# Kernel tuning notes

Hardware: AMD Instinct MI355X
Metric: run time of the kernel (lower is better)

The kernel has to match this reference:

```python
import jax, jax.numpy as jnp
import numpy as np

EPS = 1e-6  # module eps (unused in forward math, kept for fidelity)


def _relative_transform(rot_a, trans_a, rot_b, trans_b):
    # rel_rot = R_a @ R_b^T ; rel_trans = t_a - rel_rot @ t_b
    rel_rot = jnp.einsum('bij,bkj->bik', rot_a, rot_b)          # [B,3,3]
    rel_trans = trans_a - jnp.einsum('bij,bj->bi', rel_rot, trans_b)  # [B,3]
    return rel_rot, rel_trans


def setup_inputs() -> dict:
    key = jax.random.key(0)
    ks = jax.random.split(key, 9)
    B, N = 8, 4096
    return {
        'pred_rot': jax.random.normal(ks[0], (B, 3, 3), jnp.float32),
        'pred_trans': jax.random.normal(ks[1], (B, 3), jnp.float32),
        'ctx_hyp_rot': jax.random.normal(ks[2], (B, 3, 3), jnp.float32),
        'ctx_hyp_trans': jax.random.normal(ks[3], (B, 3), jnp.float32),
        'gt_rot': jax.random.normal(ks[4], (B, 3, 3), jnp.float32),
        'gt_trans': jax.random.normal(ks[5], (B, 3), jnp.float32),
        'ctx_gt_rot': jax.random.normal(ks[6], (B, 3, 3), jnp.float32),
        'ctx_gt_trans': jax.random.normal(ks[7], (B, 3), jnp.float32),
        'model_points': jax.random.normal(ks[8], (B, N, 3), jnp.float32),
    }


def reference(pred_rot, pred_trans, ctx_hyp_rot, ctx_hyp_trans,
              gt_rot, gt_trans, ctx_gt_rot, ctx_gt_trans, model_points):
    rel_pred_rot, rel_pred_trans = _relative_transform(pred_rot, pred_trans, ctx_hyp_rot, ctx_hyp_trans)
    rel_gt_rot, rel_gt_trans = _relative_transform(gt_rot, gt_trans, ctx_gt_rot, ctx_gt_trans)

    # pts = P @ R^T + t   -> [B,N,3]
    pts_pred = jnp.einsum('bnj,bij->bni', model_points, rel_pred_rot) + rel_pred_trans[:, None, :]
    pts_gt = jnp.einsum('bnj,bij->bni', model_points, rel_gt_rot) + rel_gt_trans[:, None, :]

    # pairwise euclidean distance [B,N,M]
    sq = (jnp.sum(pts_pred**2, -1)[:, :, None]
          + jnp.sum(pts_gt**2, -1)[:, None, :]
          - 2.0 * jnp.einsum('bnd,bmd->bnm', pts_pred, pts_gt))
    dist = jnp.sqrt(jnp.maximum(sq, 0.0))

    # symmetric chamfer: mean of row-min + mean of col-min, per batch
    loss_geo = jnp.min(dist, axis=2).mean(axis=1) + jnp.min(dist, axis=1).mean(axis=1)  # [B]
    loss_trans = jnp.abs(rel_pred_trans - rel_gt_trans).mean()
    return (loss_geo.mean(), loss_trans)
```

## Files before the change

kernel.cpp:

```cpp
#include <hip/hip_runtime.h>
#include <hip/hip_bf16.h>
#include <math.h>


#define TPB 256
#define RPT 8
#define MC  128
#define RC  (TPB * RPT)

__device__ __forceinline__ unsigned f2ord(float f) {
    unsigned u = __float_as_uint(f);
    return (u & 0x80000000u) ? ~u : (u | 0x80000000u);
}
__device__ __forceinline__ float ord2f(unsigned u) {
    return (u & 0x80000000u) ? __uint_as_float(u & 0x7fffffffu)
                             : __uint_as_float(~u);
}

__device__ __forceinline__ void rel_tf(const float* __restrict__ Ra,
                                       const float* __restrict__ ta,
                                       const float* __restrict__ Rb,
                                       const float* __restrict__ tb,
                                       float* R, float* t) {
#pragma unroll
    for (int i = 0; i < 3; i++)
#pragma unroll
        for (int k = 0; k < 3; k++)
            R[i * 3 + k] = Ra[i * 3 + 0] * Rb[k * 3 + 0]
                         + Ra[i * 3 + 1] * Rb[k * 3 + 1]
                         + Ra[i * 3 + 2] * Rb[k * 3 + 2];
#pragma unroll
    for (int i = 0; i < 3; i++)
        t[i] = ta[i] - (R[i * 3 + 0] * tb[0] + R[i * 3 + 1] * tb[1]
                      + R[i * 3 + 2] * tb[2]);
}

__global__ void k_prep(const float* __restrict__ pred_rot,
                       const float* __restrict__ pred_trans,
                       const float* __restrict__ ctx_hyp_rot,
                       const float* __restrict__ ctx_hyp_trans,
                       const float* __restrict__ gt_rot,
                       const float* __restrict__ gt_trans,
                       const float* __restrict__ ctx_gt_rot,
                       const float* __restrict__ ctx_gt_trans,
                       const float* __restrict__ mp,
                       float4* __restrict__ pts,
                       unsigned* __restrict__ rowmin,
                       float* __restrict__ out, int B, int N) {
    int idx = blockIdx.x * blockDim.x + threadIdx.x;
    if (idx >= B * N) return;
    int b = idx / N;
    float px = mp[idx * 3 + 0], py = mp[idx * 3 + 1], pz = mp[idx * 3 + 2];
    float R[9], t[3];
#pragma unroll
    for (int g = 0; g < 2; g++) {
        if (g == 0)
            rel_tf(pred_rot + b * 9, pred_trans + b * 3,
                   ctx_hyp_rot + b * 9, ctx_hyp_trans + b * 3, R, t);
        else
            rel_tf(gt_rot + b * 9, gt_trans + b * 3,
                   ctx_gt_rot + b * 9, ctx_gt_trans + b * 3, R, t);
        float x = R[0] * px + R[1] * py + R[2] * pz + t[0];
        float y = R[3] * px + R[4] * py + R[5] * pz + t[1];
        float z = R[6] * px + R[7] * py + R[8] * pz + t[2];
        pts[(size_t)g * B * N + idx] = make_float4(x, y, z, x * x + y * y + z * z);
    }
    rowmin[idx] = 0xFFFFFFFFu;
    rowmin[(size_t)B * N + idx] = 0xFFFFFFFFu;
    if (idx == 0) {
        out[0] = 0.0f;
        float lt = 0.0f;
        for (int bb = 0; bb < B; bb++) {
            float Rp[9], tp[3], Rg[9], tg[3];
            rel_tf(pred_rot + bb * 9, pred_trans + bb * 3,
                   ctx_hyp_rot + bb * 9, ctx_hyp_trans + bb * 3, Rp, tp);
            rel_tf(gt_rot + bb * 9, gt_trans + bb * 3,
                   ctx_gt_rot + bb * 9, ctx_gt_trans + bb * 3, Rg, tg);
            lt += fabsf(tp[0] - tg[0]) + fabsf(tp[1] - tg[1]) + fabsf(tp[2] - tg[2]);
        }
        out[1] = lt / (float)(3 * B);
    }
}

__global__ void __launch_bounds__(TPB) k_chamfer(const float4* __restrict__ pts,
                                                 unsigned* __restrict__ rowmin,
                                                 int B, int N) {
    int dir = blockIdx.z;
    int b = blockIdx.y;
    int nMC = N / MC;
    int rc = blockIdx.x / nMC;
    int mc = blockIdx.x % nMC;
    const float4* Ap = pts + ((size_t)dir * B + b) * N;
    const float4* Bp = pts + ((size_t)(1 - dir) * B + b) * N;

    __shared__ float4 sB[MC];
    int tid = threadIdx.x;
    for (int i = tid; i < MC; i += TPB) sB[i] = Bp[mc * MC + i];

    int rowBase = rc * RC;
    float a2x[RPT], a2y[RPT], a2z[RPT], mn[RPT];
#pragma unroll
    for (int r = 0; r < RPT; r++) {
        float4 a = Ap[rowBase + tid + TPB * r];
        a2x[r] = -2.0f * a.x;
        a2y[r] = -2.0f * a.y;
        a2z[r] = -2.0f * a.z;
        mn[r] = INFINITY;
    }
    __syncthreads();

#pragma unroll 4
    for (int m = 0; m < MC; m++) {
        float4 g = sB[m];
#pragma unroll
        for (int r = 0; r < RPT; r++) {
            float p = __builtin_fmaf(a2z[r], g.z, g.w);
            p = __builtin_fmaf(a2y[r], g.y, p);
            p = __builtin_fmaf(a2x[r], g.x, p);
            mn[r] = fminf(mn[r], p);
        }
    }

#pragma unroll
    for (int r = 0; r < RPT; r++) {
        size_t idx = ((size_t)dir * B + b) * N + rowBase + tid + TPB * r;
        atomicMin(&rowmin[idx], f2ord(mn[r]));
    }
}

__global__ void k_finalize(const float4* __restrict__ pts,
                           const unsigned* __restrict__ rowmin,
                           float* __restrict__ out, int B, int N) {
    int total = 2 * B * N;
    float s = 0.0f;
    for (int i = blockIdx.x * blockDim.x + threadIdx.x; i < total;
         i += gridDim.x * blockDim.x) {
        float part = ord2f(rowmin[i]);
        float sq = fmaxf(part + pts[i].w, 0.0f);
        s += sqrtf(sq);
    }
#pragma unroll
    for (int off = 32; off > 0; off >>= 1) s += __shfl_down(s, off, 64);
    __shared__ float red[TPB / 64];
    int wid = threadIdx.x >> 6, lane = threadIdx.x & 63;
    if (lane == 0) red[wid] = s;
    __syncthreads();
    if (threadIdx.x == 0) {
        float t = 0.0f;
#pragma unroll
        for (int w = 0; w < TPB / 64; w++) t += red[w];
        atomicAdd(&out[0], t / (float)(B * N));
    }
}

extern "C" void kernel_launch(void* const* d_in, const int* in_sizes, int n_in,
                              void* d_out, int out_size, void* d_ws, size_t ws_size,
                              hipStream_t stream) {
    const float* pred_rot      = (const float*)d_in[0];
    const float* pred_trans    = (const float*)d_in[1];
    const float* ctx_hyp_rot   = (const float*)d_in[2];
    const float* ctx_hyp_trans = (const float*)d_in[3];
    const float* gt_rot        = (const float*)d_in[4];
    const float* gt_trans      = (const float*)d_in[5];
    const float* ctx_gt_rot    = (const float*)d_in[6];
    const float* ctx_gt_trans  = (const float*)d_in[7];
    const float* model_points  = (const float*)d_in[8];

    int B = in_sizes[0] / 9;
    int N = in_sizes[8] / (3 * B);

    char* ws = (char*)d_ws;
    float4*   pts    = (float4*)ws;
    unsigned* rowmin = (unsigned*)(ws + (size_t)2 * B * N * 16);
    float*    out    = (float*)d_out;

    k_prep<<<(B * N + TPB - 1) / TPB, TPB, 0, stream>>>(
        pred_rot, pred_trans, ctx_hyp_rot, ctx_hyp_trans,
        gt_rot, gt_trans, ctx_gt_rot, ctx_gt_trans,
        model_points, pts, rowmin, out, B, N);

    dim3 grid((N / RC) * (N / MC), B, 2);
    k_chamfer<<<grid, TPB, 0, stream>>>(pts, rowmin, B, N);

    k_finalize<<<128, TPB, 0, stream>>>(pts, rowmin, out, B, N);
}
```

Before: 97.21 us.

## Fuse both chamfer directions into one pass with row and column partial minima

Each pairwise distance tile is now computed once and reduced both ways. Row minima stay in registers, while column minima are reduced across the wavefront with xor shuffles and across waves in shared memory. This removes the duplicate second-direction pass and the atomicMin on order-encoded floats. Per-tile partial minima are written to workspace buffers and combined in the finalize kernel. The cost is extra shuffle traffic per column pair, a smaller column tile, and a larger partial buffer that finalize must read.

```diff
diff --git a/kernel.cpp b/kernel.cpp
--- a/kernel.cpp
+++ b/kernel.cpp
@@ -1,21 +1,11 @@
 #include <hip/hip_runtime.h>
-#include <hip/hip_bf16.h>
 #include <math.h>
 
 
 #define TPB 256
 #define RPT 8
-#define MC  128
+#define MC  64
 #define RC  (TPB * RPT)
-
-__device__ __forceinline__ unsigned f2ord(float f) {
-    unsigned u = __float_as_uint(f);
-    return (u & 0x80000000u) ? ~u : (u | 0x80000000u);
-}
-__device__ __forceinline__ float ord2f(unsigned u) {
-    return (u & 0x80000000u) ? __uint_as_float(u & 0x7fffffffu)
-                             : __uint_as_float(~u);
-}
 
 __device__ __forceinline__ void rel_tf(const float* __restrict__ Ra,
                                        const float* __restrict__ ta,
@@ -45,7 +35,6 @@
                        const float* __restrict__ ctx_gt_trans,
                        const float* __restrict__ mp,
                        float4* __restrict__ pts,
-                       unsigned* __restrict__ rowmin,
                        float* __restrict__ out, int B, int N) {
     int idx = blockIdx.x * blockDim.x + threadIdx.x;
     if (idx >= B * N) return;
@@ -65,8 +54,6 @@
         float z = R[6] * px + R[7] * py + R[8] * pz + t[2];
         pts[(size_t)g * B * N + idx] = make_float4(x, y, z, x * x + y * y + z * z);
     }
-    rowmin[idx] = 0xFFFFFFFFu;
-    rowmin[(size_t)B * N + idx] = 0xFFFFFFFFu;
     if (idx == 0) {
         out[0] = 0.0f;
         float lt = 0.0f;
@@ -82,62 +69,96 @@
     }
 }
 
-__global__ void __launch_bounds__(TPB) k_chamfer(const float4* __restrict__ pts,
-                                                 unsigned* __restrict__ rowmin,
-                                                 int B, int N) {
-    int dir = blockIdx.z;
-    int b = blockIdx.y;
+__global__ void __launch_bounds__(TPB, 4)
+k_fused(const float4* __restrict__ pts,
+        float* __restrict__ rowp, float* __restrict__ colp, int B, int N) {
     int nMC = N / MC;
+    int b  = blockIdx.y;
     int rc = blockIdx.x / nMC;
     int mc = blockIdx.x % nMC;
-    const float4* Ap = pts + ((size_t)dir * B + b) * N;
-    const float4* Bp = pts + ((size_t)(1 - dir) * B + b) * N;
-
-    __shared__ float4 sB[MC];
+    size_t BN = (size_t)B * N;
+    const float4* Ap = pts + (size_t)b * N;
+    const float4* Gp = pts + BN + (size_t)b * N;
+
+    __shared__ float4 sG[MC];
+    __shared__ float cmw[TPB / 64][MC];
     int tid = threadIdx.x;
-    for (int i = tid; i < MC; i += TPB) sB[i] = Bp[mc * MC + i];
+    if (tid < MC) sG[tid] = Gp[mc * MC + tid];
 
     int rowBase = rc * RC;
-    float a2x[RPT], a2y[RPT], a2z[RPT], mn[RPT];
+    float a2x[RPT], a2y[RPT], a2z[RPT], aw[RPT], mn[RPT];
 #pragma unroll
     for (int r = 0; r < RPT; r++) {
         float4 a = Ap[rowBase + tid + TPB * r];
         a2x[r] = -2.0f * a.x;
         a2y[r] = -2.0f * a.y;
         a2z[r] = -2.0f * a.z;
-        mn[r] = INFINITY;
+        aw[r]  = a.w;
+        mn[r]  = INFINITY;
     }
     __syncthreads();
 
-#pragma unroll 4
-    for (int m = 0; m < MC; m++) {
-        float4 g = sB[m];
+    int wid = tid >> 6, lane = tid & 63;
+#pragma unroll 2
+    for (int m = 0; m < MC; m += 2) {
+        float4 g0 = sG[m];
+        float4 g1 = sG[m + 1];
+        float c0, c1;
 #pragma unroll
         for (int r = 0; r < RPT; r++) {
-            float p = __builtin_fmaf(a2z[r], g.z, g.w);
-            p = __builtin_fmaf(a2y[r], g.y, p);
-            p = __builtin_fmaf(a2x[r], g.x, p);
-            mn[r] = fminf(mn[r], p);
-        }
-    }
-
-#pragma unroll
-    for (int r = 0; r < RPT; r++) {
-        size_t idx = ((size_t)dir * B + b) * N + rowBase + tid + TPB * r;
-        atomicMin(&rowmin[idx], f2ord(mn[r]));
-    }
-}
-
-__global__ void k_finalize(const float4* __restrict__ pts,
-                           const unsigned* __restrict__ rowmin,
-                           float* __restrict__ out, int B, int N) {
-    int total = 2 * B * N;
+            float p0 = __builtin_fmaf(a2z[r], g0.z, g0.w);
+            p0 = __builtin_fmaf(a2y[r], g0.y, p0);
+            p0 = __builtin_fmaf(a2x[r], g0.x, p0);
+            float p1 = __builtin_fmaf(a2z[r], g1.z, g1.w);
+            p1 = __builtin_fmaf(a2y[r], g1.y, p1);
+            p1 = __builtin_fmaf(a2x[r], g1.x, p1);
+            float d0 = p0 + aw[r];
+            float d1 = p1 + aw[r];
+            mn[r] = fminf(fminf(mn[r], d0), d1);
+            c0 = (r == 0) ? d0 : fminf(c0, d0);
+            c1 = (r == 0) ? d1 : fminf(c1, d1);
+        }
+#pragma unroll
+        for (int off = 1; off < 64; off <<= 1) {
+            c0 = fminf(c0, __shfl_xor(c0, off, 64));
+            c1 = fminf(c1, __shfl_xor(c1, off, 64));
+        }
+        if (lane == 0) { cmw[wid][m] = c0; cmw[wid][m + 1] = c1; }
+    }
+
+    float* rp = rowp + (size_t)mc * BN + (size_t)b * N + rowBase + tid;
+#pragma unroll
+    for (int r = 0; r < RPT; r++) rp[(size_t)TPB * r] = mn[r];
+
+    __syncthreads();
+    if (tid < MC) {
+        float c = fminf(fminf(cmw[0][tid], cmw[1][tid]),
+                        fminf(cmw[2][tid], cmw[3][tid]));
+        colp[(size_t)rc * BN + (size_t)b * N + mc * MC + tid] = c;
+    }
+}
+
+__global__ void __launch_bounds__(TPB)
+k_finalize(const float* __restrict__ rowp, const float* __restrict__ colp,
+           float* __restrict__ out, int B, int N, int nMC, int nRC) {
+    size_t BN = (size_t)B * N;
+    int total = 2 * (int)BN;
     float s = 0.0f;
     for (int i = blockIdx.x * blockDim.x + threadIdx.x; i < total;
          i += gridDim.x * blockDim.x) {
-        float part = ord2f(rowmin[i]);
-        float sq = fmaxf(part + pts[i].w, 0.0f);
-        s += sqrtf(sq);
+        const float* src;
+        int cnt;
+        size_t off;
+        if (i < (int)BN) { src = rowp; cnt = nMC; off = (size_t)i; }
+        else             { src = colp; cnt = nRC; off = (size_t)i - BN; }
+        float m0 = src[off];
+        float m1 = src[BN + off];
+        for (int k = 2; k + 1 < cnt; k += 2) {
+            m0 = fminf(m0, src[(size_t)k * BN + off]);
+            m1 = fminf(m1, src[(size_t)(k + 1) * BN + off]);
+        }
+        float m = fminf(m0, m1);
+        s += sqrtf(fmaxf(m, 0.0f));
     }
 #pragma unroll
     for (int off = 32; off > 0; off >>= 1) s += __shfl_down(s, off, 64);
@@ -168,19 +189,23 @@
 
     int B = in_sizes[0] / 9;
     int N = in_sizes[8] / (3 * B);
+    size_t BN = (size_t)B * N;
+    int nMC = N / MC;
+    int nRC = N / RC;
 
     char* ws = (char*)d_ws;
-    float4*   pts    = (float4*)ws;
-    unsigned* rowmin = (unsigned*)(ws + (size_t)2 * B * N * 16);
-    float*    out    = (float*)d_out;
+    float4* pts  = (float4*)ws;
+    float*  rowp = (float*)(ws + 2 * BN * sizeof(float4));
+    float*  colp = rowp + (size_t)nMC * BN;
+    float*  out  = (float*)d_out;
 
     k_prep<<<(B * N + TPB - 1) / TPB, TPB, 0, stream>>>(
         pred_rot, pred_trans, ctx_hyp_rot, ctx_hyp_trans,
         gt_rot, gt_trans, ctx_gt_rot, ctx_gt_trans,
-        model_points, pts, rowmin, out, B, N);
-
-    dim3 grid((N / RC) * (N / MC), B, 2);
-    k_chamfer<<<grid, TPB, 0, stream>>>(pts, rowmin, B, N);
-
-    k_finalize<<<128, TPB, 0, stream>>>(pts, rowmin, out, B, N);
-}
+        model_points, pts, out, B, N);
+
+    dim3 grid(nRC * nMC, B);
+    k_fused<<<grid, TPB, 0, stream>>>(pts, rowp, colp, B, N);
+
+    k_finalize<<<128, TPB, 0, stream>>>(rowp, colp, out, B, N, nMC, nRC);
+}
```

New measurement: 113.1 us. 1.16x slower.

## Use packed FMA and min3 in chamfer loop, replace atomics with partial-min buffer

Applied to the files above, without the earlier changes.

The inner distance loop now uses v_pk_fma_f32 to evaluate two columns per instruction and v_min3_f32 to fold both into the running minimum. The -2 scaling moves to the shared column tile, which is stored as structure-of-arrays. Per-row atomicMin on order-preserving uints is replaced by writing a partial minimum per column chunk to a workspace buffer, which the finalize kernel reduces. This removes atomics and the rowmin initialization, at the cost of a much larger workspace (nMC x 2BN floats) and more finalize reads.

```diff
diff --git a/kernel.cpp b/kernel.cpp
--- a/kernel.cpp
+++ b/kernel.cpp
@@ -1,5 +1,4 @@
 #include <hip/hip_runtime.h>
-#include <hip/hip_bf16.h>
 #include <math.h>
 
 
@@ -8,13 +7,17 @@
 #define MC  128
 #define RC  (TPB * RPT)
 
-__device__ __forceinline__ unsigned f2ord(float f) {
-    unsigned u = __float_as_uint(f);
-    return (u & 0x80000000u) ? ~u : (u | 0x80000000u);
-}
-__device__ __forceinline__ float ord2f(unsigned u) {
-    return (u & 0x80000000u) ? __uint_as_float(u & 0x7fffffffu)
-                             : __uint_as_float(~u);
+typedef float f32x2 __attribute__((ext_vector_type(2)));
+
+__device__ __forceinline__ f32x2 pk_fma(f32x2 a, f32x2 b, f32x2 c) {
+    f32x2 d;
+    asm("v_pk_fma_f32 %0, %1, %2, %3" : "=v"(d) : "v"(a), "v"(b), "v"(c));
+    return d;
+}
+__device__ __forceinline__ float min3f(float a, float b, float c) {
+    float d;
+    asm("v_min3_f32 %0, %1, %2, %3" : "=v"(d) : "v"(a), "v"(b), "v"(c));
+    return d;
 }
 
 __device__ __forceinline__ void rel_tf(const float* __restrict__ Ra,
@@ -45,7 +48,6 @@
                        const float* __restrict__ ctx_gt_trans,
                        const float* __restrict__ mp,
                        float4* __restrict__ pts,
-                       unsigned* __restrict__ rowmin,
                        float* __restrict__ out, int B, int N) {
     int idx = blockIdx.x * blockDim.x + threadIdx.x;
     if (idx >= B * N) return;
@@ -65,8 +67,6 @@
         float z = R[6] * px + R[7] * py + R[8] * pz + t[2];
         pts[(size_t)g * B * N + idx] = make_float4(x, y, z, x * x + y * y + z * z);
     }
-    rowmin[idx] = 0xFFFFFFFFu;
-    rowmin[(size_t)B * N + idx] = 0xFFFFFFFFu;
     if (idx == 0) {
         out[0] = 0.0f;
         float lt = 0.0f;
@@ -82,62 +82,78 @@
     }
 }
 
-__global__ void __launch_bounds__(TPB) k_chamfer(const float4* __restrict__ pts,
-                                                 unsigned* __restrict__ rowmin,
-                                                 int B, int N) {
+__global__ void __launch_bounds__(TPB, 4)
+k_chamfer(const float4* __restrict__ pts, float* __restrict__ rowp,
+          int B, int N) {
     int dir = blockIdx.z;
     int b = blockIdx.y;
     int nMC = N / MC;
     int rc = blockIdx.x / nMC;
     int mc = blockIdx.x % nMC;
+    size_t BN = (size_t)B * N;
     const float4* Ap = pts + ((size_t)dir * B + b) * N;
-    const float4* Bp = pts + ((size_t)(1 - dir) * B + b) * N;
-
-    __shared__ float4 sB[MC];
+    const float4* Gp = pts + ((size_t)(1 - dir) * B + b) * N;
+
+    __shared__ __align__(16) float sGx[MC], sGy[MC], sGz[MC], sGw[MC];
     int tid = threadIdx.x;
-    for (int i = tid; i < MC; i += TPB) sB[i] = Bp[mc * MC + i];
+    if (tid < MC) {
+        float4 g = Gp[mc * MC + tid];
+        sGx[tid] = -2.0f * g.x;
+        sGy[tid] = -2.0f * g.y;
+        sGz[tid] = -2.0f * g.z;
+        sGw[tid] = g.w;
+    }
 
     int rowBase = rc * RC;
-    float a2x[RPT], a2y[RPT], a2z[RPT], mn[RPT];
+    f32x2 ax2[RPT], ay2[RPT], az2[RPT];
+    float mn[RPT];
 #pragma unroll
     for (int r = 0; r < RPT; r++) {
         float4 a = Ap[rowBase + tid + TPB * r];
-        a2x[r] = -2.0f * a.x;
-        a2y[r] = -2.0f * a.y;
-        a2z[r] = -2.0f * a.z;
+        ax2[r] = f32x2{a.x, a.x};
+        ay2[r] = f32x2{a.y, a.y};
+        az2[r] = f32x2{a.z, a.z};
         mn[r] = INFINITY;
     }
     __syncthreads();
 
-#pragma unroll 4
-    for (int m = 0; m < MC; m++) {
-        float4 g = sB[m];
+    const f32x2* gx2 = (const f32x2*)sGx;
+    const f32x2* gy2 = (const f32x2*)sGy;
+    const f32x2* gz2 = (const f32x2*)sGz;
+    const f32x2* gw2 = (const f32x2*)sGw;
+#pragma unroll 2
+    for (int m = 0; m < MC / 2; m++) {
+        f32x2 gx = gx2[m], gy = gy2[m], gz = gz2[m], gw = gw2[m];
 #pragma unroll
         for (int r = 0; r < RPT; r++) {
-            float p = __builtin_fmaf(a2z[r], g.z, g.w);
-            p = __builtin_fmaf(a2y[r], g.y, p);
-            p = __builtin_fmaf(a2x[r], g.x, p);
-            mn[r] = fminf(mn[r], p);
+            f32x2 p = pk_fma(az2[r], gz, gw);
+            p = pk_fma(ay2[r], gy, p);
+            p = pk_fma(ax2[r], gx, p);
+            mn[r] = min3f(mn[r], p.x, p.y);
         }
     }
 
-#pragma unroll
-    for (int r = 0; r < RPT; r++) {
-        size_t idx = ((size_t)dir * B + b) * N + rowBase + tid + TPB * r;
-        atomicMin(&rowmin[idx], f2ord(mn[r]));
-    }
-}
-
-__global__ void k_finalize(const float4* __restrict__ pts,
-                           const unsigned* __restrict__ rowmin,
-                           float* __restrict__ out, int B, int N) {
-    int total = 2 * B * N;
+    float* rp = rowp + (size_t)mc * 2 * BN
+              + (size_t)dir * BN + (size_t)b * N + rowBase + tid;
+#pragma unroll
+    for (int r = 0; r < RPT; r++) rp[(size_t)TPB * r] = mn[r];
+}
+
+__global__ void __launch_bounds__(TPB)
+k_finalize(const float4* __restrict__ pts, const float* __restrict__ rowp,
+           float* __restrict__ out, int B, int N, int nMC) {
+    size_t BN2 = (size_t)2 * B * N;
     float s = 0.0f;
-    for (int i = blockIdx.x * blockDim.x + threadIdx.x; i < total;
-         i += gridDim.x * blockDim.x) {
-        float part = ord2f(rowmin[i]);
-        float sq = fmaxf(part + pts[i].w, 0.0f);
-        s += sqrtf(sq);
+    for (size_t i = blockIdx.x * blockDim.x + threadIdx.x; i < BN2;
+         i += (size_t)gridDim.x * blockDim.x) {
+        float m0 = rowp[i];
+        float m1 = rowp[BN2 + i];
+        for (int k = 2; k + 1 < nMC; k += 2) {
+            m0 = fminf(m0, rowp[(size_t)k * BN2 + i]);
+            m1 = fminf(m1, rowp[(size_t)(k + 1) * BN2 + i]);
+        }
+        float m = fminf(m0, m1);
+        s += sqrtf(fmaxf(m + pts[i].w, 0.0f));
     }
 #pragma unroll
     for (int off = 32; off > 0; off >>= 1) s += __shfl_down(s, off, 64);
@@ -168,19 +184,22 @@
 
     int B = in_sizes[0] / 9;
     int N = in_sizes[8] / (3 * B);
+    size_t BN = (size_t)B * N;
+    int nMC = N / MC;
+    int nRC = N / RC;
 
     char* ws = (char*)d_ws;
-    float4*   pts    = (float4*)ws;
-    unsigned* rowmin = (unsigned*)(ws + (size_t)2 * B * N * 16);
-    float*    out    = (float*)d_out;
+    float4* pts  = (float4*)ws;
+    float*  rowp = (float*)(ws + 2 * BN * sizeof(float4));
+    float*  out  = (float*)d_out;
 
     k_prep<<<(B * N + TPB - 1) / TPB, TPB, 0, stream>>>(
         pred_rot, pred_trans, ctx_hyp_rot, ctx_hyp_trans,
         gt_rot, gt_trans, ctx_gt_rot, ctx_gt_trans,
-        model_points, pts, rowmin, out, B, N);
-
-    dim3 grid((N / RC) * (N / MC), B, 2);
-    k_chamfer<<<grid, TPB, 0, stream>>>(pts, rowmin, B, N);
-
-    k_finalize<<<128, TPB, 0, stream>>>(pts, rowmin, out, B, N);
-}
+        model_points, pts, out, B, N);
+
+    dim3 grid(nRC * nMC, B, 2);
+    k_chamfer<<<grid, TPB, 0, stream>>>(pts, rowp, B, N);
+
+    k_finalize<<<128, TPB, 0, stream>>>(pts, rowp, out, B, N, nMC);
+}
```

Result: slower. 106.1 us (+9.2%).

## Compute chamfer distances with bf16 split-precision MFMA and fuse min/finalize

Applied to the files above, without the earlier changes.

Recasts the pairwise squared-distance computation as a matrix product on MFMA units. Each coordinate is split into bf16 hi/lo parts so the dot product keeps near-fp32 accuracy, with the squared norm folded in as an extra K column. Each wave owns a 32-row strip, scans all columns through shared memory, and reduces row minima in registers. This removes the atomicMin scatter and the separate finalize kernel, and the sqrt/sum is folded into the same kernel. The cost is extra prep work and some residual precision loss from the 3-term bf16 split. The chamfer kernel's grid also shrinks to fewer, larger blocks.

```diff
diff --git a/kernel.cpp b/kernel.cpp
--- a/kernel.cpp
+++ b/kernel.cpp
@@ -1,20 +1,27 @@
 #include <hip/hip_runtime.h>
-#include <hip/hip_bf16.h>
 #include <math.h>
 
 
-#define TPB 256
-#define RPT 8
-#define MC  128
-#define RC  (TPB * RPT)
-
-__device__ __forceinline__ unsigned f2ord(float f) {
-    unsigned u = __float_as_uint(f);
-    return (u & 0x80000000u) ? ~u : (u | 0x80000000u);
-}
-__device__ __forceinline__ float ord2f(unsigned u) {
-    return (u & 0x80000000u) ? __uint_as_float(u & 0x7fffffffu)
-                             : __uint_as_float(~u);
+#define PTPB 256
+#define CW   8
+
+typedef __attribute__((ext_vector_type(8)))  short bf16x8;
+typedef __attribute__((ext_vector_type(16))) float f32x16;
+
+__device__ __forceinline__ unsigned short f2bf(float x) {
+    unsigned u = __float_as_uint(x);
+    return (unsigned short)((u + 0x7FFFu + ((u >> 16) & 1u)) >> 16);
+}
+__device__ __forceinline__ float bf2f(unsigned short h) {
+    return __uint_as_float(((unsigned)h) << 16);
+}
+__device__ __forceinline__ uint4 pack8(const unsigned short v[8]) {
+    uint4 r;
+    r.x = (unsigned)v[0] | ((unsigned)v[1] << 16);
+    r.y = (unsigned)v[2] | ((unsigned)v[3] << 16);
+    r.z = (unsigned)v[4] | ((unsigned)v[5] << 16);
+    r.w = (unsigned)v[6] | ((unsigned)v[7] << 16);
+    return r;
 }
 
 __device__ __forceinline__ void rel_tf(const float* __restrict__ Ra,
@@ -44,29 +51,54 @@
                        const float* __restrict__ ctx_gt_rot,
                        const float* __restrict__ ctx_gt_trans,
                        const float* __restrict__ mp,
-                       float4* __restrict__ pts,
-                       unsigned* __restrict__ rowmin,
+                       uint4* __restrict__ Arow, uint4* __restrict__ Bcol,
+                       float* __restrict__ pw,
                        float* __restrict__ out, int B, int N) {
     int idx = blockIdx.x * blockDim.x + threadIdx.x;
     if (idx >= B * N) return;
-    int b = idx / N;
+    int b = idx / N, n = idx % N;
+    int T = N >> 5;
+    int tile = n >> 5, ln = n & 31;
     float px = mp[idx * 3 + 0], py = mp[idx * 3 + 1], pz = mp[idx * 3 + 2];
-    float R[9], t[3];
-#pragma unroll
-    for (int g = 0; g < 2; g++) {
-        if (g == 0)
+    const unsigned short one = 0x3F80;
+    float Rm[9], tv[3];
+#pragma unroll
+    for (int s = 0; s < 2; s++) {
+        if (s == 0)
             rel_tf(pred_rot + b * 9, pred_trans + b * 3,
-                   ctx_hyp_rot + b * 9, ctx_hyp_trans + b * 3, R, t);
+                   ctx_hyp_rot + b * 9, ctx_hyp_trans + b * 3, Rm, tv);
         else
             rel_tf(gt_rot + b * 9, gt_trans + b * 3,
-                   ctx_gt_rot + b * 9, ctx_gt_trans + b * 3, R, t);
-        float x = R[0] * px + R[1] * py + R[2] * pz + t[0];
-        float y = R[3] * px + R[4] * py + R[5] * pz + t[1];
-        float z = R[6] * px + R[7] * py + R[8] * pz + t[2];
-        pts[(size_t)g * B * N + idx] = make_float4(x, y, z, x * x + y * y + z * z);
-    }
-    rowmin[idx] = 0xFFFFFFFFu;
-    rowmin[(size_t)B * N + idx] = 0xFFFFFFFFu;
+                   ctx_gt_rot + b * 9, ctx_gt_trans + b * 3, Rm, tv);
+        float x = Rm[0] * px + Rm[1] * py + Rm[2] * pz + tv[0];
+        float y = Rm[3] * px + Rm[4] * py + Rm[5] * pz + tv[1];
+        float z = Rm[6] * px + Rm[7] * py + Rm[8] * pz + tv[2];
+        float w = x * x + y * y + z * z;
+
+        float mx = -2.0f * x, my = -2.0f * y, mz = -2.0f * z;
+        unsigned short ahx = f2bf(mx), ahy = f2bf(my), ahz = f2bf(mz);
+        unsigned short alx = f2bf(mx - bf2f(ahx));
+        unsigned short aly = f2bf(my - bf2f(ahy));
+        unsigned short alz = f2bf(mz - bf2f(ahz));
+        unsigned short ghx = f2bf(x), ghy = f2bf(y), ghz = f2bf(z);
+        unsigned short glx = f2bf(x - bf2f(ghx));
+        unsigned short gly = f2bf(y - bf2f(ghy));
+        unsigned short glz = f2bf(z - bf2f(ghz));
+        unsigned short gwh = f2bf(w);
+        unsigned short gwl = f2bf(w - bf2f(gwh));
+
+        unsigned short a_lo[8] = {ahx, ahy, ahz, alx, aly, alz, ahx, ahy};
+        unsigned short a_hi[8] = {ahz, alx, aly, alz, one, one, 0, 0};
+        unsigned short b_lo[8] = {ghx, ghy, ghz, ghx, ghy, ghz, glx, gly};
+        unsigned short b_hi[8] = {glz, glx, gly, glz, gwh, gwl, 0, 0};
+
+        size_t base = (((size_t)s * B + b) * T + tile) * 64;
+        Arow[base + ln]      = pack8(a_lo);
+        Arow[base + 32 + ln] = pack8(a_hi);
+        Bcol[base + ln]      = pack8(b_lo);
+        Bcol[base + 32 + ln] = pack8(b_hi);
+        pw[((size_t)s * B + b) * N + n] = w;
+    }
     if (idx == 0) {
         out[0] = 0.0f;
         float lt = 0.0f;
@@ -82,74 +114,76 @@
     }
 }
 
-__global__ void __launch_bounds__(TPB) k_chamfer(const float4* __restrict__ pts,
-                                                 unsigned* __restrict__ rowmin,
-                                                 int B, int N) {
-    int dir = blockIdx.z;
-    int b = blockIdx.y;
-    int nMC = N / MC;
-    int rc = blockIdx.x / nMC;
-    int mc = blockIdx.x % nMC;
-    const float4* Ap = pts + ((size_t)dir * B + b) * N;
-    const float4* Bp = pts + ((size_t)(1 - dir) * B + b) * N;
-
-    __shared__ float4 sB[MC];
-    int tid = threadIdx.x;
-    for (int i = tid; i < MC; i += TPB) sB[i] = Bp[mc * MC + i];
-
-    int rowBase = rc * RC;
-    float a2x[RPT], a2y[RPT], a2z[RPT], mn[RPT];
-#pragma unroll
-    for (int r = 0; r < RPT; r++) {
-        float4 a = Ap[rowBase + tid + TPB * r];
-        a2x[r] = -2.0f * a.x;
-        a2y[r] = -2.0f * a.y;
-        a2z[r] = -2.0f * a.z;
-        mn[r] = INFINITY;
-    }
+__global__ void __launch_bounds__(CW * 64)
+k_mfma(const uint4* __restrict__ Arow, const uint4* __restrict__ Bcol,
+       const float* __restrict__ pw, float* __restrict__ out, int B, int N) {
+    int T = N >> 5;
+    int pass = blockIdx.z, b = blockIdx.y;
+    int tid = threadIdx.x, wid = tid >> 6, lane = tid & 63;
+    int strip = blockIdx.x * CW + wid;
+
+    const uint4* Ap  = Arow + ((size_t)pass * B + b) * T * 64;
+    const uint4* Bs  = Bcol + ((size_t)(1 - pass) * B + b) * T * 64;
+    const float* pwp = pw + ((size_t)pass * B + b) * N;
+
+    __shared__ uint4 sB[CW][64];
+
+    uint4 au = Ap[(size_t)strip * 64 + lane];
+    bf16x8 af = *(bf16x8*)&au;
+
+    f32x16 rmin;
+#pragma unroll
+    for (int r = 0; r < 16; r++) rmin[r] = INFINITY;
+    f32x16 zc;
+#pragma unroll
+    for (int r = 0; r < 16; r++) zc[r] = 0.0f;
+
+    uint4 stg = Bs[(size_t)wid * 64 + lane];
+    int nchunk = T / CW;
+    for (int c = 0; c < nchunk; c++) {
+        __syncthreads();
+        sB[wid][lane] = stg;
+        if (c + 1 < nchunk)
+            stg = Bs[(((size_t)(c + 1)) * CW + wid) * 64 + lane];
+        __syncthreads();
+#pragma unroll
+        for (int t = 0; t < CW; t++) {
+            uint4 bu = sB[t][lane];
+            bf16x8 bf = *(bf16x8*)&bu;
+            f32x16 d = __builtin_amdgcn_mfma_f32_32x32x16_bf16(af, bf, zc, 0, 0, 0);
+#pragma unroll
+            for (int r = 0; r < 16; r++) rmin[r] = fminf(rmin[r], d[r]);
+        }
+    }
+
+#pragma unroll
+    for (int off = 1; off < 32; off <<= 1) {
+#pragma unroll
+        for (int r = 0; r < 16; r++)
+            rmin[r] = fminf(rmin[r], __shfl_xor(rmin[r], off, 64));
+    }
+
+    float lsum = 0.0f;
+    if ((lane & 31) == 0) {
+        int h = lane >> 5;
+        int rowbase = strip * 32;
+#pragma unroll
+        for (int r = 0; r < 16; r++) {
+            int row = (r & 3) + 8 * (r >> 2) + 4 * h;
+            float v = rmin[r] + pwp[rowbase + row];
+            lsum += sqrtf(fmaxf(v, 0.0f));
+        }
+    }
+    lsum += __shfl_down(lsum, 32, 64);
+
+    __shared__ float red[CW];
+    if (lane == 0) red[wid] = lsum;
     __syncthreads();
-
-#pragma unroll 4
-    for (int m = 0; m < MC; m++) {
-        float4 g = sB[m];
-#pragma unroll
-        for (int r = 0; r < RPT; r++) {
-            float p = __builtin_fmaf(a2z[r], g.z, g.w);
-            p = __builtin_fmaf(a2y[r], g.y, p);
-            p = __builtin_fmaf(a2x[r], g.x, p);
-            mn[r] = fminf(mn[r], p);
-        }
-    }
-
-#pragma unroll
-    for (int r = 0; r < RPT; r++) {
-        size_t idx = ((size_t)dir * B + b) * N + rowBase + tid + TPB * r;
-        atomicMin(&rowmin[idx], f2ord(mn[r]));
-    }
-}
-
-__global__ void k_finalize(const float4* __restrict__ pts,
-                           const unsigned* __restrict__ rowmin,
-                           float* __restrict__ out, int B, int N) {
-    int total = 2 * B * N;
-    float s = 0.0f;
-    for (int i = blockIdx.x * blockDim.x + threadIdx.x; i < total;
-         i += gridDim.x * blockDim.x) {
-        float part = ord2f(rowmin[i]);
-        float sq = fmaxf(part + pts[i].w, 0.0f);
-        s += sqrtf(sq);
-    }
-#pragma unroll
-    for (int off = 32; off > 0; off >>= 1) s += __shfl_down(s, off, 64);
-    __shared__ float red[TPB / 64];
-    int wid = threadIdx.x >> 6, lane = threadIdx.x & 63;
-    if (lane == 0) red[wid] = s;
-    __syncthreads();
-    if (threadIdx.x == 0) {
-        float t = 0.0f;
-#pragma unroll
-        for (int w = 0; w < TPB / 64; w++) t += red[w];
-        atomicAdd(&out[0], t / (float)(B * N));
+    if (tid == 0) {
+        float tsum = 0.0f;
+#pragma unroll
+        for (int w = 0; w < CW; w++) tsum += red[w];
+        atomicAdd(&out[0], tsum / (float)(B * N));
     }
 }
 
@@ -168,19 +202,20 @@
 
     int B = in_sizes[0] / 9;
     int N = in_sizes[8] / (3 * B);
+    int T = N >> 5;
+    size_t fragN = (size_t)2 * B * T * 64;
 
     char* ws = (char*)d_ws;
-    float4*   pts    = (float4*)ws;
-    unsigned* rowmin = (unsigned*)(ws + (size_t)2 * B * N * 16);
-    float*    out    = (float*)d_out;
-
-    k_prep<<<(B * N + TPB - 1) / TPB, TPB, 0, stream>>>(
+    uint4* Arow = (uint4*)ws;
+    uint4* Bcol = Arow + fragN;
+    float* pw   = (float*)(Bcol + fragN);
+    float* out  = (float*)d_out;
+
+    k_prep<<<(B * N + PTPB - 1) / PTPB, PTPB, 0, stream>>>(
         pred_rot, pred_trans, ctx_hyp_rot, ctx_hyp_trans,
         gt_rot, gt_trans, ctx_gt_rot, ctx_gt_trans,
-        model_points, pts, rowmin, out, B, N);
-
-    dim3 grid((N / RC) * (N / MC), B, 2);
-    k_chamfer<<<grid, TPB, 0, stream>>>(pts, rowmin, B, N);
-
-    k_finalize<<<128, TPB, 0, stream>>>(pts, rowmin, out, B, N);
-}
+        model_points, Arow, Bcol, pw, out, B, N);
+
+    dim3 grid(N / (CW * 32), B, 2);
+    k_mfma<<<grid, CW * 64, 0, stream>>>(Arow, Bcol, pw, out, B, N);
+}
```

After: 92.47 us, median of 2. -4.9%, faster.
